# Kernel tuning notes

Hardware: AMD Instinct MI355X
Metric: run time of the kernel (lower is better)

## Reference

```python
import jax, jax.numpy as jnp
import numpy as np

DIM = 512
HEADS = 8
BLOCKS = 6
DFF = 2048
B = 4
T = 2048
VOCAB = 20
CLASSES = 1
MAX_TOKENS = 5000
EPS = 1e-5


def _make_pe():
    # Sinusoidal positional encoding, identical to PositionalEncodingSin
    pos = np.arange(MAX_TOKENS, dtype=np.float32)[:, None]
    div = np.exp(np.arange(0, DIM, 2, dtype=np.float32) * (-np.log(10000.0) / DIM))
    pe = np.zeros((MAX_TOKENS, DIM), dtype=np.float32)
    pe[:, 0::2] = np.sin(pos * div)
    pe[:, 1::2] = np.cos(pos * div)
    return jnp.asarray(pe)


def setup_inputs() -> dict:
    key = jax.random.key(0)
    ks = jax.random.split(key, 8)

    def n(k, shape, s=0.02):
        return (jax.random.normal(k, shape) * s).astype(jnp.float32)

    x = jax.random.randint(ks[0], (B, T), 0, VOCAB, dtype=jnp.int32)
    embed = n(ks[1], (VOCAB, DIM))
    pe = _make_pe()
    Wqkv = n(ks[2], (BLOCKS, DIM, 3 * DIM))   # to_qvk (no bias)
    W0 = n(ks[3], (BLOCKS, DIM, DIM))          # W_0 (no bias)
    g1 = jnp.ones((BLOCKS, DIM), jnp.float32)
    b1 = jnp.zeros((BLOCKS, DIM), jnp.float32)
    g2 = jnp.ones((BLOCKS, DIM), jnp.float32)
    b2 = jnp.zeros((BLOCKS, DIM), jnp.float32)
    Wl1 = n(ks[4], (BLOCKS, DIM, DFF))
    bl1 = jnp.zeros((BLOCKS, DFF), jnp.float32)
    Wl2 = n(ks[5], (BLOCKS, DFF, DIM))
    bl2 = jnp.zeros((BLOCKS, DIM), jnp.float32)
    Whead = n(ks[6], (DIM, CLASSES))
    bhead = jnp.zeros((CLASSES,), jnp.float32)
    return dict(x=x, embed=embed, pe=pe, Wqkv=Wqkv, W0=W0, g1=g1, b1=b1,
                g2=g2, b2=b2, Wl1=Wl1, bl1=bl1, Wl2=Wl2, bl2=bl2,
                Whead=Whead, bhead=bhead)


def _ln(x, g, b):
    mu = x.mean(-1, keepdims=True)
    var = ((x - mu) ** 2).mean(-1, keepdims=True)
    return (x - mu) / jnp.sqrt(var + EPS) * g + b


def _mhsa(x, Wqkv, W0):
    b, t, _ = x.shape
    dh = DIM // HEADS
    qkv = x @ Wqkv                                   # [b, t, 3*DIM]
    # rearrange 'b t (d k h) -> k b h t d' with k=3, h=HEADS
    qkv = qkv.reshape(b, t, dh, 3, HEADS).transpose(3, 0, 4, 1, 2)
    q, k, v = qkv[0], qkv[1], qkv[2]                 # [b, h, t, dh]
    scores = jnp.einsum('bhid,bhjd->bhij', q, k) * (dh ** -0.5)
    attn = jax.nn.softmax(scores, axis=-1)
    out = jnp.einsum('bhij,bhjd->bhid', attn, v)
    out = out.transpose(0, 2, 1, 3).reshape(b, t, DIM)  # 'b h t d -> b t (h d)'
    return out @ W0


def _forward(x, embed, pe, Wqkv, W0, g1, b1, g2, b2, Wl1, bl1, Wl2, bl2, Whead, bhead):
    h = embed[x] + pe[None, :x.shape[1], :]          # embedding + sinusoidal PE (dropout off)
    for i in range(BLOCKS):                          # post-norm transformer blocks
        a = _mhsa(h, Wqkv[i], W0[i])
        y = _ln(a + h, g1[i], b1[i])
        m = jax.nn.gelu(y @ Wl1[i] + bl1[i], approximate=False) @ Wl2[i] + bl2[i]
        h = _ln(m + y, g2[i], b2[i])
    return (h @ Whead + bhead).squeeze(-1)           # [B, T]


def reference(x, embed, pe, Wqkv, W0, g1, b1, g2, b2, Wl1, bl1, Wl2, bl2, Whead, bhead):
    return _forward(x, embed, pe, Wqkv, W0, g1, b1, g2, b2, Wl1, bl1, Wl2, bl2, Whead, bhead)
```

## Files before the change

### kernel.cpp

```cpp
#include <hip/hip_runtime.h>
#include <hip/hip_bf16.h>
#include <math.h>

#define DIMD 512
#define HEADS 8
#define NBLK 6
#define DFF 2048
#define BATCH 4
#define SEQ 2048
#define NTOK 8192
#define DH 64
#define LNEPS 1e-5f
#define QSCALE 0.1803368801111204f

typedef __bf16 bf16;
typedef __bf16 bf16x8 __attribute__((ext_vector_type(8)));
typedef __bf16 bf16x4 __attribute__((ext_vector_type(4)));
typedef float f32x4 __attribute__((ext_vector_type(4)));

__device__ __forceinline__ void async16(const void* g, void* l) {
  __builtin_amdgcn_global_load_lds(
      (const __attribute__((address_space(1))) void*)g,
      (__attribute__((address_space(3))) void*)l, 16, 0, 0);
}

__global__ void k_cvt_t(const float* __restrict__ in, bf16* __restrict__ out, int K, int N) {
  __shared__ float T[32][33];
  const float* src = in + (size_t)blockIdx.z * K * N;
  bf16* dst = out + (size_t)blockIdx.z * K * N;
  int k0 = blockIdx.y * 32, n0 = blockIdx.x * 32;
  int r = threadIdx.x >> 3, c4 = (threadIdx.x & 7) * 4;
  float4 v = *reinterpret_cast<const float4*>(src + (size_t)(k0 + r) * N + n0 + c4);
  T[r][c4] = v.x; T[r][c4 + 1] = v.y; T[r][c4 + 2] = v.z; T[r][c4 + 3] = v.w;
  __syncthreads();
  bf16x4 o;
  o[0] = (bf16)T[c4][r]; o[1] = (bf16)T[c4 + 1][r];
  o[2] = (bf16)T[c4 + 2][r]; o[3] = (bf16)T[c4 + 3][r];
  *reinterpret_cast<bf16x4*>(dst + (size_t)(n0 + r) * K + k0 + c4) = o;
}

__global__ void k_cvt_qkv(const float* __restrict__ in, bf16* __restrict__ out, int K, int N) {
  __shared__ float T[32][33];
  const float* src = in + (size_t)blockIdx.z * K * N;
  bf16* dst = out + (size_t)blockIdx.z * K * N;
  int k0 = blockIdx.y * 32, n0 = blockIdx.x * 32;
  int r = threadIdx.x >> 3, c4 = (threadIdx.x & 7) * 4;
  float4 v = *reinterpret_cast<const float4*>(src + (size_t)(k0 + r) * N + n0 + c4);
  T[r][c4] = v.x; T[r][c4 + 1] = v.y; T[r][c4 + 2] = v.z; T[r][c4 + 3] = v.w;
  __syncthreads();
  int n_src = n0 + r;
  int d = n_src / 24;
  int rem = n_src - d * 24;
  int np = (rem >> 3) * 512 + (rem & 7) * 64 + d;
  bf16x4 o;
  o[0] = (bf16)T[c4][r]; o[1] = (bf16)T[c4 + 1][r];
  o[2] = (bf16)T[c4 + 2][r]; o[3] = (bf16)T[c4 + 3][r];
  *reinterpret_cast<bf16x4*>(dst + (size_t)np * K + k0 + c4) = o;
}

__global__ void k_embed(const int* __restrict__ x, const float* __restrict__ embed,
                        const float* __restrict__ pe, bf16* __restrict__ hb,
                        float* __restrict__ hf) {
  int row = blockIdx.x;
  int t = row & (SEQ - 1);
  int tok = x[row];
  int c = threadIdx.x * 2;
  const float* e = embed + (size_t)tok * DIMD;
  const float* p = pe + (size_t)t * DIMD;
  float v0 = e[c] + p[c];
  float v1 = e[c + 1] + p[c + 1];
  size_t o = (size_t)row * DIMD + c;
  hb[o] = (bf16)v0; hb[o + 1] = (bf16)v1;
  hf[o] = v0;       hf[o + 1] = v1;
}

enum { EPI_QKV = 0, EPI_RES = 1, EPI_GELU = 2, EPI_BIASRES = 3 };

template <int EPI>
__global__ __launch_bounds__(256) void k_gemm(
    const bf16* __restrict__ A, const bf16* __restrict__ Wt,
    const float* __restrict__ bias, const float* __restrict__ resf,
    bf16* __restrict__ out0, bf16* __restrict__ out1, bf16* __restrict__ out2,
    float* __restrict__ outf, int N, int K) {
  __shared__ bf16 As[128][32];
  __shared__ bf16 Bs[128][32];
  int tid = threadIdx.x;
  int w = tid >> 6, lane = tid & 63, quad = lane >> 4, l15 = lane & 15;
  int m0 = blockIdx.y * 128, n0 = blockIdx.x * 128;
  int wr = w >> 1, wc = w & 1;

  int srow = w * 32 + (lane >> 2);
  int sw = (((lane & 3) ^ ((lane >> 3) & 3))) * 8;
  const bf16* Ag = A + (size_t)(m0 + srow) * K + sw;
  const bf16* Bg = Wt + (size_t)(n0 + srow) * K + sw;
  bf16* AsU = &As[0][0] + (size_t)w * 1024;
  bf16* BsU = &Bs[0][0] + (size_t)w * 1024;

  int fcol = (quad ^ ((l15 >> 1) & 3)) * 8;

  f32x4 acc[4][4] = {};

  for (int k0 = 0; k0 < K; k0 += 32) {
    async16(Ag + k0, AsU);
    async16(Ag + k0 + (size_t)16 * K, AsU + 512);
    async16(Bg + k0, BsU);
    async16(Bg + k0 + (size_t)16 * K, BsU + 512);
    __syncthreads();

    bf16x8 af[4], bfr[4];
#pragma unroll
    for (int i = 0; i < 4; ++i)
      af[i] = *reinterpret_cast<const bf16x8*>(&As[wr * 64 + i * 16 + l15][fcol]);
#pragma unroll
    for (int j = 0; j < 4; ++j)
      bfr[j] = *reinterpret_cast<const bf16x8*>(&Bs[wc * 64 + j * 16 + l15][fcol]);
#pragma unroll
    for (int i = 0; i < 4; ++i)
#pragma unroll
      for (int j = 0; j < 4; ++j)
        acc[i][j] = __builtin_amdgcn_mfma_f32_16x16x32_bf16(af[i], bfr[j], acc[i][j], 0, 0, 0);
    __syncthreads();
  }

#pragma unroll
  for (int j = 0; j < 4; ++j) {
    int col = n0 + wc * 64 + j * 16 + l15;
    int qwhich = 0, qhh = 0, qdd = 0;
    float bcol = 0.f;
    if (EPI == EPI_QKV) {
      qwhich = col >> 9;
      qhh = (col >> 6) & 7;
      qdd = col & 63;
    } else if (EPI == EPI_GELU || EPI == EPI_BIASRES) {
      bcol = bias[col];
    }
#pragma unroll
    for (int i = 0; i < 4; ++i) {
#pragma unroll
      for (int r = 0; r < 4; ++r) {
        int row = m0 + wr * 64 + i * 16 + quad * 4 + r;
        float v = acc[i][j][r];
        if (EPI == EPI_QKV) {
          int b = row >> 11;
          int t = row & (SEQ - 1);
          int bh = b * HEADS + qhh;
          if (qwhich == 0)      out0[((size_t)bh * SEQ + t) * DH + qdd] = (bf16)(v * QSCALE);
          else if (qwhich == 1) out1[((size_t)bh * SEQ + t) * DH + qdd] = (bf16)v;
          else                  out2[((size_t)bh * DH + qdd) * SEQ + t] = (bf16)v;
        } else if (EPI == EPI_RES) {
          outf[(size_t)row * N + col] = v + resf[(size_t)row * N + col];
        } else if (EPI == EPI_GELU) {
          float xv = v + bcol;
          out0[(size_t)row * N + col] = (bf16)(0.5f * xv * (1.0f + erff(xv * 0.70710678118f)));
        } else {
          outf[(size_t)row * N + col] = v + bcol + resf[(size_t)row * N + col];
        }
      }
    }
  }
}

__global__ __launch_bounds__(256) void k_attn(const bf16* __restrict__ q,
                                              const bf16* __restrict__ k,
                                              const bf16* __restrict__ vt,
                                              bf16* __restrict__ out) {
  __shared__ bf16 Ks[64][64];
  __shared__ bf16 Vs[64][64];
  __shared__ bf16 Pw[4][16][72];
  int tid = threadIdx.x;
  int w = tid >> 6, lane = tid & 63, quad = lane >> 4, l15 = lane & 15;
  int qt = blockIdx.x, bh = blockIdx.y;
  const bf16* qbase = q + (size_t)bh * SEQ * DH;
  const bf16* kbase = k + (size_t)bh * SEQ * DH;
  const bf16* vbase = vt + (size_t)bh * DH * SEQ;

  int qrow = qt * 64 + w * 16 + l15;
  bf16x8 qf[2];
  qf[0] = *reinterpret_cast<const bf16x8*>(qbase + (size_t)qrow * DH + quad * 8);
  qf[1] = *reinterpret_cast<const bf16x8*>(qbase + (size_t)qrow * DH + 32 + quad * 8);

  int strow = w * 16 + (lane >> 3);
  int scol = ((lane & 7) ^ (lane >> 3)) * 8;
  const bf16* kp = kbase + (size_t)strow * DH + scol;
  const bf16* vp = vbase + (size_t)strow * SEQ + scol;
  bf16* kdst = &Ks[0][0] + (size_t)w * 1024 + (size_t)lane * 8;
  bf16* vdst = &Vs[0][0] + (size_t)w * 1024 + (size_t)lane * 8;

  f32x4 Ot[4] = {};
  float ls = 0.f;
  int fx = (l15 & 7);

  bf16x8 ka = *reinterpret_cast<const bf16x8*>(kp);
  bf16x8 kb = *reinterpret_cast<const bf16x8*>(kp + (size_t)8 * DH);
  bf16x8 va = *reinterpret_cast<const bf16x8*>(vp);
  bf16x8 vb = *reinterpret_cast<const bf16x8*>(vp + (size_t)8 * SEQ);
  kp += (size_t)64 * DH;

  for (int j0 = 0; j0 < SEQ; j0 += 64) {
    __syncthreads();
    *reinterpret_cast<bf16x8*>(kdst) = ka;
    *reinterpret_cast<bf16x8*>(kdst + 512) = kb;
    *reinterpret_cast<bf16x8*>(vdst) = va;
    *reinterpret_cast<bf16x8*>(vdst + 512) = vb;
    __syncthreads();
    if (j0 + 64 < SEQ) {
      ka = *reinterpret_cast<const bf16x8*>(kp);
      kb = *reinterpret_cast<const bf16x8*>(kp + (size_t)8 * DH);
      va = *reinterpret_cast<const bf16x8*>(vp + j0 + 64);
      vb = *reinterpret_cast<const bf16x8*>(vp + j0 + 64 + (size_t)8 * SEQ);
      kp += (size_t)64 * DH;
    }

    f32x4 st[4];
#pragma unroll
    for (int nt = 0; nt < 4; ++nt) {
      bf16x8 kf0 = *reinterpret_cast<const bf16x8*>(&Ks[nt * 16 + l15][(quad ^ fx) * 8]);
      bf16x8 kf1 = *reinterpret_cast<const bf16x8*>(&Ks[nt * 16 + l15][((quad + 4) ^ fx) * 8]);
      f32x4 z = {};
      z = __builtin_amdgcn_mfma_f32_16x16x32_bf16(kf0, qf[0], z, 0, 0, 0);
      z = __builtin_amdgcn_mfma_f32_16x16x32_bf16(kf1, qf[1], z, 0, 0, 0);
      st[nt] = z;
    }

#pragma unroll
    for (int nt = 0; nt < 4; ++nt) {
#pragma unroll
      for (int r = 0; r < 4; ++r) {
        float p = exp2f(st[nt][r]);
        st[nt][r] = p;
        ls += p;
      }
      bf16x4 pv;
      pv[0] = (bf16)st[nt][0]; pv[1] = (bf16)st[nt][1];
      pv[2] = (bf16)st[nt][2]; pv[3] = (bf16)st[nt][3];
      *reinterpret_cast<bf16x4*>(&Pw[w][l15][nt * 16 + quad * 4]) = pv;
    }

#pragma unroll
    for (int h = 0; h < 2; ++h) {
      bf16x8 pf = *reinterpret_cast<const bf16x8*>(&Pw[w][l15][h * 32 + quad * 8]);
#pragma unroll
      for (int nt = 0; nt < 4; ++nt) {
        bf16x8 vf = *reinterpret_cast<const bf16x8*>(&Vs[nt * 16 + l15][((quad + 4 * h) ^ fx) * 8]);
        Ot[nt] = __builtin_amdgcn_mfma_f32_16x16x32_bf16(vf, pf, Ot[nt], 0, 0, 0);
      }
    }
  }

  ls += __shfl_xor(ls, 16);
  ls += __shfl_xor(ls, 32);
  float inv = 1.0f / ls;
#pragma unroll
  for (int nt = 0; nt < 4; ++nt) {
    bf16x4 ov;
    ov[0] = (bf16)(Ot[nt][0] * inv); ov[1] = (bf16)(Ot[nt][1] * inv);
    ov[2] = (bf16)(Ot[nt][2] * inv); ov[3] = (bf16)(Ot[nt][3] * inv);
    *reinterpret_cast<bf16x4*>(&Pw[w][l15][nt * 16 + quad * 4]) = ov;
  }
  int qr = lane >> 2, c0 = (lane & 3) * 16;
  bf16x8 o0 = *reinterpret_cast<const bf16x8*>(&Pw[w][qr][c0]);
  bf16x8 o1 = *reinterpret_cast<const bf16x8*>(&Pw[w][qr][c0 + 8]);
  int b = bh >> 3, hh = bh & 7;
  int token = b * SEQ + qt * 64 + w * 16 + qr;
  *reinterpret_cast<bf16x8*>(out + (size_t)token * DIMD + hh * DH + c0) = o0;
  *reinterpret_cast<bf16x8*>(out + (size_t)token * DIMD + hh * DH + c0 + 8) = o1;
}

__global__ void k_ln(const float* __restrict__ in, const float* __restrict__ g,
                     const float* __restrict__ b, bf16* __restrict__ outb,
                     float* __restrict__ outf) {
  int wid = (blockIdx.x * blockDim.x + threadIdx.x) >> 6;
  int lane = threadIdx.x & 63;
  const float* row = in + (size_t)wid * DIMD;
  float4 x0 = *reinterpret_cast<const float4*>(row + lane * 8);
  float4 x1 = *reinterpret_cast<const float4*>(row + lane * 8 + 4);
  float xs[8] = {x0.x, x0.y, x0.z, x0.w, x1.x, x1.y, x1.z, x1.w};
  float s = 0.f, sq = 0.f;
#pragma unroll
  for (int j = 0; j < 8; ++j) { s += xs[j]; sq += xs[j] * xs[j]; }
#pragma unroll
  for (int m = 1; m < 64; m <<= 1) { s += __shfl_xor(s, m); sq += __shfl_xor(sq, m); }
  float mu = s * (1.0f / DIMD);
  float var = sq * (1.0f / DIMD) - mu * mu;
  float rstd = rsqrtf(var + LNEPS);
  bf16x8 ov;
#pragma unroll
  for (int j = 0; j < 8; ++j) {
    int c = lane * 8 + j;
    float y = (xs[j] - mu) * rstd * g[c] + b[c];
    ov[j] = (bf16)y;
    outf[(size_t)wid * DIMD + c] = y;
  }
  *reinterpret_cast<bf16x8*>(outb + (size_t)wid * DIMD + lane * 8) = ov;
}

__global__ void k_head(const bf16* __restrict__ h, const float* __restrict__ w,
                       const float* __restrict__ bh, float* __restrict__ out) {
  int row = (blockIdx.x * blockDim.x + threadIdx.x) >> 6;
  int lane = threadIdx.x & 63;
  bf16x8 xv = *reinterpret_cast<const bf16x8*>(h + (size_t)row * DIMD + lane * 8);
  float s = 0.f;
#pragma unroll
  for (int j = 0; j < 8; ++j) s += (float)xv[j] * w[lane * 8 + j];
#pragma unroll
  for (int m = 1; m < 64; m <<= 1) s += __shfl_xor(s, m);
  if (lane == 0) out[row] = s + bh[0];
}

extern "C" void kernel_launch(void* const* d_in, const int* in_sizes, int n_in,
                              void* d_out, int out_size, void* d_ws, size_t ws_size,
                              hipStream_t stream) {
  const int*   x     = (const int*)d_in[0];
  const float* embed = (const float*)d_in[1];
  const float* pe    = (const float*)d_in[2];
  const float* Wqkv  = (const float*)d_in[3];
  const float* W0    = (const float*)d_in[4];
  const float* g1    = (const float*)d_in[5];
  const float* b1    = (const float*)d_in[6];
  const float* g2    = (const float*)d_in[7];
  const float* b2    = (const float*)d_in[8];
  const float* Wl1   = (const float*)d_in[9];
  const float* bl1   = (const float*)d_in[10];
  const float* Wl2   = (const float*)d_in[11];
  const float* bl2   = (const float*)d_in[12];
  const float* Whead = (const float*)d_in[13];
  const float* bhead = (const float*)d_in[14];
  float* outp = (float*)d_out;

  char* ws = (char*)d_ws;
  size_t off = 0;
  auto alloc = [&](size_t bytes) { void* p = ws + off; off += (bytes + 255) & ~(size_t)255; return p; };
  const size_t ACT = (size_t)NTOK * DIMD;
  bf16*  hb   = (bf16*)alloc(ACT * 2);
  float* hf   = (float*)alloc(ACT * 4);
  bf16*  qb   = (bf16*)alloc(ACT * 2);
  bf16*  kb   = (bf16*)alloc(ACT * 2);
  bf16*  vtb  = (bf16*)alloc(ACT * 2);
  bf16*  ao   = (bf16*)alloc(ACT * 2);
  float* r32  = (float*)alloc(ACT * 4);
  bf16*  yb   = (bf16*)alloc(ACT * 2);
  float* yf   = (float*)alloc(ACT * 4);
  bf16*  wqkt = (bf16*)alloc((size_t)NBLK * DIMD * 3 * DIMD * 2);
  bf16*  w0t  = (bf16*)alloc((size_t)NBLK * DIMD * DIMD * 2);
  bf16*  wl1t = (bf16*)alloc((size_t)NBLK * DIMD * DFF * 2);
  bf16*  wl2t = (bf16*)alloc((size_t)NBLK * DFF * DIMD * 2);
  bf16*  mid  = qb;

  k_cvt_qkv<<<dim3(3 * DIMD / 32, DIMD / 32, NBLK), 256, 0, stream>>>(Wqkv, wqkt, DIMD, 3 * DIMD);
  k_cvt_t<<<dim3(DIMD / 32, DIMD / 32, NBLK), 256, 0, stream>>>(W0, w0t, DIMD, DIMD);
  k_cvt_t<<<dim3(DFF / 32, DIMD / 32, NBLK), 256, 0, stream>>>(Wl1, wl1t, DIMD, DFF);
  k_cvt_t<<<dim3(DIMD / 32, DFF / 32, NBLK), 256, 0, stream>>>(Wl2, wl2t, DFF, DIMD);

  k_embed<<<NTOK, 256, 0, stream>>>(x, embed, pe, hb, hf);
  for (int i = 0; i < NBLK; ++i) {
    k_gemm<EPI_QKV><<<dim3(3 * DIMD / 128, NTOK / 128), 256, 0, stream>>>(
        hb, wqkt + (size_t)i * DIMD * 3 * DIMD, nullptr, nullptr,
        qb, kb, vtb, nullptr, 3 * DIMD, DIMD);
    k_attn<<<dim3(SEQ / 64, BATCH * HEADS), 256, 0, stream>>>(qb, kb, vtb, ao);
    k_gemm<EPI_RES><<<dim3(DIMD / 128, NTOK / 128), 256, 0, stream>>>(
        ao, w0t + (size_t)i * DIMD * DIMD, nullptr, hf,
        nullptr, nullptr, nullptr, r32, DIMD, DIMD);
    k_ln<<<NTOK / 4, 256, 0, stream>>>(r32, g1 + i * DIMD, b1 + i * DIMD, yb, yf);
    k_gemm<EPI_GELU><<<dim3(DFF / 128, NTOK / 128), 256, 0, stream>>>(
        yb, wl1t + (size_t)i * DIMD * DFF, bl1 + (size_t)i * DFF, nullptr,
        mid, nullptr, nullptr, nullptr, DFF, DIMD);
    k_gemm<EPI_BIASRES><<<dim3(DIMD / 128, NTOK / 128), 256, 0, stream>>>(
        mid, wl2t + (size_t)i * DFF * DIMD, bl2 + (size_t)i * DIMD, yf,
        nullptr, nullptr, nullptr, r32, DIMD, DFF);
    k_ln<<<NTOK / 4, 256, 0, stream>>>(r32, g2 + i * DIMD, b2 + i * DIMD, hb, hf);
  }
  k_head<<<NTOK / 4, 256, 0, stream>>>(hb, Whead, bhead, outp);
}
```

Before: 1.480 ms.

## Switch GEMMs to 32x32 MFMA, add 64-row tiles, double attention query rows

The GEMM kernel moves from 16x16x32 to 32x32x16 bf16 MFMA with a new swizzle, which cuts LDS fragment reads per MFMA. It also gains a 64-row tile variant, used for the two N=512 GEMMs so more blocks fill the GPU. The attention kernel now handles 128 query rows per block (two 64-row sets per wave) and reuses each loaded K/V tile twice, halving K/V traffic. This raises register pressure and leaves the attention grid at 512 blocks.

Result: faster. 1.390 ms (-6.1%).

```diff
diff --git a/kernel.cpp b/kernel.cpp
--- a/kernel.cpp
+++ b/kernel.cpp
@@ -17,12 +17,15 @@
 typedef __bf16 bf16x8 __attribute__((ext_vector_type(8)));
 typedef __bf16 bf16x4 __attribute__((ext_vector_type(4)));
 typedef float f32x4 __attribute__((ext_vector_type(4)));
+typedef float f32x16 __attribute__((ext_vector_type(16)));
 
 __device__ __forceinline__ void async16(const void* g, void* l) {
   __builtin_amdgcn_global_load_lds(
       (const __attribute__((address_space(1))) void*)g,
       (__attribute__((address_space(3))) void*)l, 16, 0, 0);
 }
+
+__device__ __forceinline__ int swz(int r) { return ((r >> 1) ^ (r >> 3)) & 3; }
 
 __global__ void k_cvt_t(const float* __restrict__ in, bf16* __restrict__ out, int K, int N) {
   __shared__ float T[32][33];
@@ -76,70 +79,97 @@
 
 enum { EPI_QKV = 0, EPI_RES = 1, EPI_GELU = 2, EPI_BIASRES = 3 };
 
-template <int EPI>
+template <int EPI, int MT>
 __global__ __launch_bounds__(256) void k_gemm(
     const bf16* __restrict__ A, const bf16* __restrict__ Wt,
     const float* __restrict__ bias, const float* __restrict__ resf,
     bf16* __restrict__ out0, bf16* __restrict__ out1, bf16* __restrict__ out2,
     float* __restrict__ outf, int N, int K) {
-  __shared__ bf16 As[128][32];
+  constexpr int TJ = (MT == 128) ? 2 : 1;
+  __shared__ bf16 As[MT][32];
   __shared__ bf16 Bs[128][32];
   int tid = threadIdx.x;
-  int w = tid >> 6, lane = tid & 63, quad = lane >> 4, l15 = lane & 15;
-  int m0 = blockIdx.y * 128, n0 = blockIdx.x * 128;
-  int wr = w >> 1, wc = w & 1;
-
-  int srow = w * 32 + (lane >> 2);
-  int sw = (((lane & 3) ^ ((lane >> 3) & 3))) * 8;
-  const bf16* Ag = A + (size_t)(m0 + srow) * K + sw;
-  const bf16* Bg = Wt + (size_t)(n0 + srow) * K + sw;
-  bf16* AsU = &As[0][0] + (size_t)w * 1024;
-  bf16* BsU = &Bs[0][0] + (size_t)w * 1024;
-
-  int fcol = (quad ^ ((l15 >> 1) & 3)) * 8;
-
-  f32x4 acc[4][4] = {};
+  int w = tid >> 6, lane = tid & 63, hi = lane >> 5, l31 = lane & 31;
+  int m0 = blockIdx.y * MT, n0 = blockIdx.x * 128;
+  int wr = (MT == 128) ? (w >> 1) : 0;
+  int wc = (MT == 128) ? (w & 1) : w;
+
+  const bf16 *Ag0, *Ag1 = nullptr, *Bg0, *Bg1;
+  bf16 *dA0, *dA1 = nullptr, *dB0, *dB1;
+  if (MT == 128) {
+    int ra0 = w * 32 + (lane >> 2), ra1 = ra0 + 16;
+    Ag0 = A + (size_t)(m0 + ra0) * K + ((lane & 3) ^ swz(ra0)) * 8;
+    Ag1 = A + (size_t)(m0 + ra1) * K + ((lane & 3) ^ swz(ra1)) * 8;
+    Bg0 = Wt + (size_t)(n0 + ra0) * K + ((lane & 3) ^ swz(ra0)) * 8;
+    Bg1 = Wt + (size_t)(n0 + ra1) * K + ((lane & 3) ^ swz(ra1)) * 8;
+    dA0 = &As[0][0] + w * 1024; dA1 = dA0 + 512;
+    dB0 = &Bs[0][0] + w * 1024; dB1 = dB0 + 512;
+  } else {
+    int ra = w * 16 + (lane >> 2);
+    Ag0 = A + (size_t)(m0 + ra) * K + ((lane & 3) ^ swz(ra)) * 8;
+    int rb0 = w * 16 + (lane >> 2), rb1 = rb0 + 64;
+    Bg0 = Wt + (size_t)(n0 + rb0) * K + ((lane & 3) ^ swz(rb0)) * 8;
+    Bg1 = Wt + (size_t)(n0 + rb1) * K + ((lane & 3) ^ swz(rb1)) * 8;
+    dA0 = &As[0][0] + w * 512;
+    dB0 = &Bs[0][0] + w * 512; dB1 = dB0 + 2048;
+  }
+
+  int rowA[2], fA[2], colB[2], fB[2];
+#pragma unroll
+  for (int i = 0; i < 2; ++i) {
+    rowA[i] = ((MT == 128) ? wr * 64 : 0) + i * 32 + l31;
+    fA[i] = swz(rowA[i]);
+  }
+#pragma unroll
+  for (int j = 0; j < TJ; ++j) {
+    colB[j] = ((MT == 128) ? (wc * 64 + j * 32) : (wc * 32)) + l31;
+    fB[j] = swz(colB[j]);
+  }
+
+  f32x16 acc[2][TJ] = {};
 
   for (int k0 = 0; k0 < K; k0 += 32) {
-    async16(Ag + k0, AsU);
-    async16(Ag + k0 + (size_t)16 * K, AsU + 512);
-    async16(Bg + k0, BsU);
-    async16(Bg + k0 + (size_t)16 * K, BsU + 512);
+    async16(Ag0 + k0, dA0);
+    if (MT == 128) async16(Ag1 + k0, dA1);
+    async16(Bg0 + k0, dB0);
+    async16(Bg1 + k0, dB1);
     __syncthreads();
 
-    bf16x8 af[4], bfr[4];
-#pragma unroll
-    for (int i = 0; i < 4; ++i)
-      af[i] = *reinterpret_cast<const bf16x8*>(&As[wr * 64 + i * 16 + l15][fcol]);
-#pragma unroll
-    for (int j = 0; j < 4; ++j)
-      bfr[j] = *reinterpret_cast<const bf16x8*>(&Bs[wc * 64 + j * 16 + l15][fcol]);
-#pragma unroll
-    for (int i = 0; i < 4; ++i)
-#pragma unroll
-      for (int j = 0; j < 4; ++j)
-        acc[i][j] = __builtin_amdgcn_mfma_f32_16x16x32_bf16(af[i], bfr[j], acc[i][j], 0, 0, 0);
+#pragma unroll
+    for (int s = 0; s < 2; ++s) {
+      int lc = s * 2 + hi;
+      bf16x8 af[2], bfr[TJ];
+#pragma unroll
+      for (int i = 0; i < 2; ++i)
+        af[i] = *reinterpret_cast<const bf16x8*>(&As[rowA[i]][(lc ^ fA[i]) * 8]);
+#pragma unroll
+      for (int j = 0; j < TJ; ++j)
+        bfr[j] = *reinterpret_cast<const bf16x8*>(&Bs[colB[j]][(lc ^ fB[j]) * 8]);
+#pragma unroll
+      for (int i = 0; i < 2; ++i)
+#pragma unroll
+        for (int j = 0; j < TJ; ++j)
+          acc[i][j] = __builtin_amdgcn_mfma_f32_32x32x16_bf16(af[i], bfr[j], acc[i][j], 0, 0, 0);
+    }
     __syncthreads();
   }
 
 #pragma unroll
-  for (int j = 0; j < 4; ++j) {
-    int col = n0 + wc * 64 + j * 16 + l15;
+  for (int j = 0; j < TJ; ++j) {
+    int col = n0 + ((MT == 128) ? (wc * 64 + j * 32) : (wc * 32)) + l31;
     int qwhich = 0, qhh = 0, qdd = 0;
     float bcol = 0.f;
     if (EPI == EPI_QKV) {
-      qwhich = col >> 9;
-      qhh = (col >> 6) & 7;
-      qdd = col & 63;
+      qwhich = col >> 9; qhh = (col >> 6) & 7; qdd = col & 63;
     } else if (EPI == EPI_GELU || EPI == EPI_BIASRES) {
       bcol = bias[col];
     }
 #pragma unroll
-    for (int i = 0; i < 4; ++i) {
-#pragma unroll
-      for (int r = 0; r < 4; ++r) {
-        int row = m0 + wr * 64 + i * 16 + quad * 4 + r;
-        float v = acc[i][j][r];
+    for (int i = 0; i < 2; ++i) {
+#pragma unroll
+      for (int reg = 0; reg < 16; ++reg) {
+        int row = m0 + ((MT == 128) ? wr * 64 : 0) + i * 32 + (reg & 3) + 8 * (reg >> 2) + 4 * hi;
+        float v = acc[i][j][reg];
         if (EPI == EPI_QKV) {
           int b = row >> 11;
           int t = row & (SEQ - 1);
@@ -166,7 +196,7 @@
                                               bf16* __restrict__ out) {
   __shared__ bf16 Ks[64][64];
   __shared__ bf16 Vs[64][64];
-  __shared__ bf16 Pw[4][16][72];
+  __shared__ bf16 Pw[4][2][16][72];
   int tid = threadIdx.x;
   int w = tid >> 6, lane = tid & 63, quad = lane >> 4, l15 = lane & 15;
   int qt = blockIdx.x, bh = blockIdx.y;
@@ -174,10 +204,13 @@
   const bf16* kbase = k + (size_t)bh * SEQ * DH;
   const bf16* vbase = vt + (size_t)bh * DH * SEQ;
 
-  int qrow = qt * 64 + w * 16 + l15;
-  bf16x8 qf[2];
-  qf[0] = *reinterpret_cast<const bf16x8*>(qbase + (size_t)qrow * DH + quad * 8);
-  qf[1] = *reinterpret_cast<const bf16x8*>(qbase + (size_t)qrow * DH + 32 + quad * 8);
+  bf16x8 qf[2][2];
+#pragma unroll
+  for (int s = 0; s < 2; ++s) {
+    int qrow = qt * 128 + s * 64 + w * 16 + l15;
+    qf[s][0] = *reinterpret_cast<const bf16x8*>(qbase + (size_t)qrow * DH + quad * 8);
+    qf[s][1] = *reinterpret_cast<const bf16x8*>(qbase + (size_t)qrow * DH + 32 + quad * 8);
+  }
 
   int strow = w * 16 + (lane >> 3);
   int scol = ((lane & 7) ^ (lane >> 3)) * 8;
@@ -186,8 +219,8 @@
   bf16* kdst = &Ks[0][0] + (size_t)w * 1024 + (size_t)lane * 8;
   bf16* vdst = &Vs[0][0] + (size_t)w * 1024 + (size_t)lane * 8;
 
-  f32x4 Ot[4] = {};
-  float ls = 0.f;
+  f32x4 Ot[2][4] = {};
+  float ls[2] = {0.f, 0.f};
   int fx = (l15 & 7);
 
   bf16x8 ka = *reinterpret_cast<const bf16x8*>(kp);
@@ -211,59 +244,70 @@
       kp += (size_t)64 * DH;
     }
 
-    f32x4 st[4];
+    f32x4 st[2][4];
 #pragma unroll
     for (int nt = 0; nt < 4; ++nt) {
       bf16x8 kf0 = *reinterpret_cast<const bf16x8*>(&Ks[nt * 16 + l15][(quad ^ fx) * 8]);
       bf16x8 kf1 = *reinterpret_cast<const bf16x8*>(&Ks[nt * 16 + l15][((quad + 4) ^ fx) * 8]);
-      f32x4 z = {};
-      z = __builtin_amdgcn_mfma_f32_16x16x32_bf16(kf0, qf[0], z, 0, 0, 0);
-      z = __builtin_amdgcn_mfma_f32_16x16x32_bf16(kf1, qf[1], z, 0, 0, 0);
-      st[nt] = z;
-    }
-
-#pragma unroll
-    for (int nt = 0; nt < 4; ++nt) {
-#pragma unroll
-      for (int r = 0; r < 4; ++r) {
-        float p = exp2f(st[nt][r]);
-        st[nt][r] = p;
-        ls += p;
+#pragma unroll
+      for (int s = 0; s < 2; ++s) {
+        f32x4 z = {};
+        z = __builtin_amdgcn_mfma_f32_16x16x32_bf16(kf0, qf[s][0], z, 0, 0, 0);
+        z = __builtin_amdgcn_mfma_f32_16x16x32_bf16(kf1, qf[s][1], z, 0, 0, 0);
+        st[s][nt] = z;
       }
-      bf16x4 pv;
-      pv[0] = (bf16)st[nt][0]; pv[1] = (bf16)st[nt][1];
-      pv[2] = (bf16)st[nt][2]; pv[3] = (bf16)st[nt][3];
-      *reinterpret_cast<bf16x4*>(&Pw[w][l15][nt * 16 + quad * 4]) = pv;
-    }
+    }
+
+#pragma unroll
+    for (int s = 0; s < 2; ++s)
+#pragma unroll
+      for (int nt = 0; nt < 4; ++nt) {
+#pragma unroll
+        for (int r = 0; r < 4; ++r) {
+          float p = exp2f(st[s][nt][r]);
+          st[s][nt][r] = p;
+          ls[s] += p;
+        }
+        bf16x4 pv;
+        pv[0] = (bf16)st[s][nt][0]; pv[1] = (bf16)st[s][nt][1];
+        pv[2] = (bf16)st[s][nt][2]; pv[3] = (bf16)st[s][nt][3];
+        *reinterpret_cast<bf16x4*>(&Pw[w][s][l15][nt * 16 + quad * 4]) = pv;
+      }
 
 #pragma unroll
     for (int h = 0; h < 2; ++h) {
-      bf16x8 pf = *reinterpret_cast<const bf16x8*>(&Pw[w][l15][h * 32 + quad * 8]);
+      bf16x8 pf0 = *reinterpret_cast<const bf16x8*>(&Pw[w][0][l15][h * 32 + quad * 8]);
+      bf16x8 pf1 = *reinterpret_cast<const bf16x8*>(&Pw[w][1][l15][h * 32 + quad * 8]);
 #pragma unroll
       for (int nt = 0; nt < 4; ++nt) {
         bf16x8 vf = *reinterpret_cast<const bf16x8*>(&Vs[nt * 16 + l15][((quad + 4 * h) ^ fx) * 8]);
-        Ot[nt] = __builtin_amdgcn_mfma_f32_16x16x32_bf16(vf, pf, Ot[nt], 0, 0, 0);
+        Ot[0][nt] = __builtin_amdgcn_mfma_f32_16x16x32_bf16(vf, pf0, Ot[0][nt], 0, 0, 0);
+        Ot[1][nt] = __builtin_amdgcn_mfma_f32_16x16x32_bf16(vf, pf1, Ot[1][nt], 0, 0, 0);
       }
     }
   }
 
-  ls += __shfl_xor(ls, 16);
-  ls += __shfl_xor(ls, 32);
-  float inv = 1.0f / ls;
-#pragma unroll
-  for (int nt = 0; nt < 4; ++nt) {
-    bf16x4 ov;
-    ov[0] = (bf16)(Ot[nt][0] * inv); ov[1] = (bf16)(Ot[nt][1] * inv);
-    ov[2] = (bf16)(Ot[nt][2] * inv); ov[3] = (bf16)(Ot[nt][3] * inv);
-    *reinterpret_cast<bf16x4*>(&Pw[w][l15][nt * 16 + quad * 4]) = ov;
-  }
+  int b = bh >> 3, hh = bh & 7;
   int qr = lane >> 2, c0 = (lane & 3) * 16;
-  bf16x8 o0 = *reinterpret_cast<const bf16x8*>(&Pw[w][qr][c0]);
-  bf16x8 o1 = *reinterpret_cast<const bf16x8*>(&Pw[w][qr][c0 + 8]);
-  int b = bh >> 3, hh = bh & 7;
-  int token = b * SEQ + qt * 64 + w * 16 + qr;
-  *reinterpret_cast<bf16x8*>(out + (size_t)token * DIMD + hh * DH + c0) = o0;
-  *reinterpret_cast<bf16x8*>(out + (size_t)token * DIMD + hh * DH + c0 + 8) = o1;
+#pragma unroll
+  for (int s = 0; s < 2; ++s) {
+    float l = ls[s];
+    l += __shfl_xor(l, 16);
+    l += __shfl_xor(l, 32);
+    float inv = 1.0f / l;
+#pragma unroll
+    for (int nt = 0; nt < 4; ++nt) {
+      bf16x4 ov;
+      ov[0] = (bf16)(Ot[s][nt][0] * inv); ov[1] = (bf16)(Ot[s][nt][1] * inv);
+      ov[2] = (bf16)(Ot[s][nt][2] * inv); ov[3] = (bf16)(Ot[s][nt][3] * inv);
+      *reinterpret_cast<bf16x4*>(&Pw[w][s][l15][nt * 16 + quad * 4]) = ov;
+    }
+    bf16x8 o0 = *reinterpret_cast<const bf16x8*>(&Pw[w][s][qr][c0]);
+    bf16x8 o1 = *reinterpret_cast<const bf16x8*>(&Pw[w][s][qr][c0 + 8]);
+    int token = b * SEQ + qt * 128 + s * 64 + w * 16 + qr;
+    *reinterpret_cast<bf16x8*>(out + (size_t)token * DIMD + hh * DH + c0) = o0;
+    *reinterpret_cast<bf16x8*>(out + (size_t)token * DIMD + hh * DH + c0 + 8) = o1;
+  }
 }
 
 __global__ void k_ln(const float* __restrict__ in, const float* __restrict__ g,
@@ -353,18 +397,18 @@
 
   k_embed<<<NTOK, 256, 0, stream>>>(x, embed, pe, hb, hf);
   for (int i = 0; i < NBLK; ++i) {
-    k_gemm<EPI_QKV><<<dim3(3 * DIMD / 128, NTOK / 128), 256, 0, stream>>>(
+    k_gemm<EPI_QKV, 128><<<dim3(3 * DIMD / 128, NTOK / 128), 256, 0, stream>>>(
         hb, wqkt + (size_t)i * DIMD * 3 * DIMD, nullptr, nullptr,
         qb, kb, vtb, nullptr, 3 * DIMD, DIMD);
-    k_attn<<<dim3(SEQ / 64, BATCH * HEADS), 256, 0, stream>>>(qb, kb, vtb, ao);
-    k_gemm<EPI_RES><<<dim3(DIMD / 128, NTOK / 128), 256, 0, stream>>>(
+    k_attn<<<dim3(SEQ / 128, BATCH * HEADS), 256, 0, stream>>>(qb, kb, vtb, ao);
+    k_gemm<EPI_RES, 64><<<dim3(DIMD / 128, NTOK / 64), 256, 0, stream>>>(
         ao, w0t + (size_t)i * DIMD * DIMD, nullptr, hf,
         nullptr, nullptr, nullptr, r32, DIMD, DIMD);
     k_ln<<<NTOK / 4, 256, 0, stream>>>(r32, g1 + i * DIMD, b1 + i * DIMD, yb, yf);
-    k_gemm<EPI_GELU><<<dim3(DFF / 128, NTOK / 128), 256, 0, stream>>>(
+    k_gemm<EPI_GELU, 128><<<dim3(DFF / 128, NTOK / 128), 256, 0, stream>>>(
         yb, wl1t + (size_t)i * DIMD * DFF, bl1 + (size_t)i * DFF, nullptr,
         mid, nullptr, nullptr, nullptr, DFF, DIMD);
-    k_gemm<EPI_BIASRES><<<dim3(DIMD / 128, NTOK / 128), 256, 0, stream>>>(
+    k_gemm<EPI_BIASRES, 64><<<dim3(DIMD / 128, NTOK / 64), 256, 0, stream>>>(
         mid, wl2t + (size_t)i * DFF * DIMD, bl2 + (size_t)i * DIMD, yf,
         nullptr, nullptr, nullptr, r32, DIMD, DFF);
     k_ln<<<NTOK / 4, 256, 0, stream>>>(r32, g2 + i * DIMD, b2 + i * DIMD, hb, hf);
```
